# Performance work log

Hardware: AMD Instinct MI355X
Metric: run time of the kernel (lower is better)

The kernel has to match this reference:

```python
import jax, jax.numpy as jnp
import numpy as np

B, N, C, L, O = 2048, 512, 64, 2, 8192  # batch, in_dim, num_candidates, lut_rank, out_dim


def setup_inputs() -> dict:
    key = jax.random.key(0)
    k1, k2, k3 = jax.random.split(key, 3)
    x = jax.random.normal(k1, (B, N), dtype=jnp.float32)
    # torch init: torch.rand(num_candidates, lut_rank, out_dim)
    weights = jax.random.uniform(k2, (C, L, O), dtype=jnp.float32)
    # connection candidates: integer indices into in_dim
    indices = jax.random.randint(k3, (C, L, O), 0, N, dtype=jnp.int64)
    return {"x": x, "weights": weights, "indices": indices}


def reference(x, weights, indices):
    # gumbel=False -> g = 0, so argmax is over raw candidate weights
    connections = jnp.argmax(weights, axis=0)           # [L, O] winning candidate per (l,o)
    l = jnp.arange(L)[:, None]                          # [L, 1]
    o = jnp.arange(O)[None, :]                          # [1, O]
    sel = indices[connections, l, o]                    # [L, O] input-feature index per (l,o)
    return x[:, sel]                                    # [B, L, O]
```

## Files before the change

kernel.cpp:

```cpp
#include <hip/hip_runtime.h>


#define BB 2048
#define NN 512
#define CC 64
#define LL 2
#define OO 8192
#define LO (LL * OO)

__global__ void sel_kernel(const float* __restrict__ weights,
                           const int* __restrict__ indices,
                           int* __restrict__ sel) {
    int t = blockIdx.x * blockDim.x + threadIdx.x;
    if (t >= LO) return;
    float best = weights[t];
    int bestc = 0;
#pragma unroll 8
    for (int c = 1; c < CC; ++c) {
        float w = weights[(size_t)c * LO + t];
        if (w > best) { best = w; bestc = c; }
    }
    sel[t] = indices[(size_t)bestc * LO + t];
}

__global__ void __launch_bounds__(256)
gather_kernel(const float* __restrict__ x,
              const int* __restrict__ sel,
              float* __restrict__ out) {
    __shared__ float xrow[NN];
    const int b = blockIdx.x;
    const float* xp = x + (size_t)b * NN;
    for (int i = threadIdx.x; i < NN; i += 256) xrow[i] = xp[i];
    __syncthreads();

    float* op = out + (size_t)b * LO;
#pragma unroll 4
    for (int i = 0; i < LO / (256 * 4); ++i) {
        int base = i * 1024 + threadIdx.x * 4;
        int4 s = *reinterpret_cast<const int4*>(sel + base);
        float4 v;
        v.x = xrow[s.x];
        v.y = xrow[s.y];
        v.z = xrow[s.z];
        v.w = xrow[s.w];
        *reinterpret_cast<float4*>(op + base) = v;
    }
}

extern "C" void kernel_launch(void* const* d_in, const int* in_sizes, int n_in,
                              void* d_out, int out_size, void* d_ws, size_t ws_size,
                              hipStream_t stream) {
    const float* x       = (const float*)d_in[0];
    const float* weights = (const float*)d_in[1];
    const int*   indices = (const int*)d_in[2];
    float*       out     = (float*)d_out;
    int*         sel     = (int*)d_ws;

    sel_kernel<<<LO / 256, 256, 0, stream>>>(weights, indices, sel);
    gather_kernel<<<BB, 256, 0, stream>>>(x, sel, out);
}
```

Measured before the change: 174.5 us.

## Tile gather over row groups and column chunks to reuse sel indices

```diff
diff --git a/kernel.cpp b/kernel.cpp
--- a/kernel.cpp
+++ b/kernel.cpp
@@ -7,6 +7,10 @@
 #define LL 2
 #define OO 8192
 #define LO (LL * OO)
+#define ROWS 8
+#define CHUNK 4096
+#define NCHUNK (LO / CHUNK)
+#define ITERS (CHUNK / (256 * 4))
 
 __global__ void sel_kernel(const float* __restrict__ weights,
                            const int* __restrict__ indices,
@@ -27,23 +31,36 @@
 gather_kernel(const float* __restrict__ x,
               const int* __restrict__ sel,
               float* __restrict__ out) {
-    __shared__ float xrow[NN];
-    const int b = blockIdx.x;
-    const float* xp = x + (size_t)b * NN;
-    for (int i = threadIdx.x; i < NN; i += 256) xrow[i] = xp[i];
+    __shared__ float xrows[ROWS * NN];
+
+    const int rg    = blockIdx.x / NCHUNK;
+    const int chunk = blockIdx.x % NCHUNK;
+    const int b0    = rg * ROWS;
+
+    const float4* xp4 = reinterpret_cast<const float4*>(x + (size_t)b0 * NN);
+    float4* sh4 = reinterpret_cast<float4*>(xrows);
+#pragma unroll
+    for (int i = 0; i < (ROWS * NN / 4) / 256; ++i)
+        sh4[i * 256 + threadIdx.x] = xp4[i * 256 + threadIdx.x];
     __syncthreads();
 
-    float* op = out + (size_t)b * LO;
-#pragma unroll 4
-    for (int i = 0; i < LO / (256 * 4); ++i) {
-        int base = i * 1024 + threadIdx.x * 4;
-        int4 s = *reinterpret_cast<const int4*>(sel + base);
-        float4 v;
-        v.x = xrow[s.x];
-        v.y = xrow[s.y];
-        v.z = xrow[s.z];
-        v.w = xrow[s.w];
-        *reinterpret_cast<float4*>(op + base) = v;
+    const int* selp = sel + chunk * CHUNK;
+    float* op = out + (size_t)b0 * LO + chunk * CHUNK;
+
+#pragma unroll
+    for (int i = 0; i < ITERS; ++i) {
+        const int base = i * 1024 + threadIdx.x * 4;
+        int4 s = *reinterpret_cast<const int4*>(selp + base);
+#pragma unroll
+        for (int r = 0; r < ROWS; ++r) {
+            const float* row = xrows + r * NN;
+            float4 v;
+            v.x = row[s.x];
+            v.y = row[s.y];
+            v.z = row[s.z];
+            v.w = row[s.w];
+            *reinterpret_cast<float4*>(op + (size_t)r * LO + base) = v;
+        }
     }
 }
 
@@ -57,5 +74,5 @@
     int*         sel     = (int*)d_ws;
 
     sel_kernel<<<LO / 256, 256, 0, stream>>>(weights, indices, sel);
-    gather_kernel<<<BB, 256, 0, stream>>>(x, sel, out);
+    gather_kernel<<<(BB / ROWS) * NCHUNK, 256, 0, stream>>>(x, sel, out);
 }
```

Result: faster. 150.9 us (median of 2 runs) (-13.6%).
